# Kernel optimization log

Measured on AMD Instinct MI355X. Metric: run time of the kernel, lower is better.

Reference implementation:

```python
import jax, jax.numpy as jnp
import numpy as np

NUM_CLASSES = 80
IMG_DIM = 2048
WORD_DIM = 300
INTER = 1024


def _branch(fmap, word, W1, W2, W3, b3, Wa, ba):
    # fmap: [B, C, H, W] -> [B, H, W, C]  (matches torch transpose(1,2),(2,3))
    x = jnp.transpose(fmap, (0, 2, 3, 1))
    fw = jnp.einsum('bhwc,dc->bhwd', x, W1)          # [B,H,W,d]
    fd = jnp.einsum('kw,dw->kd', word, W2)            # [K,d]
    # broadcast instead of repeat: tanh-gated bilinear feature [B,H,W,K,d]
    t = jnp.tanh(fw[:, :, :, None, :] * fd[None, None, None, :, :])
    lb = jnp.einsum('bhwkd,ed->bhwke', t, W3) + b3    # [B,H,W,K,d]
    score = jnp.einsum('bhwkd,od->bhwko', lb, Wa)[..., 0] + ba[0]  # [B,H,W,K]
    B, H, W, K = score.shape
    coeff = jax.nn.softmax(score.reshape(B, H * W, K), axis=1).reshape(B, H, W, K)
    # weighted spatial sum pooling per class -> [B, K, C]
    return jnp.einsum('bhwk,bhwc->bkc', coeff, x)


def setup_inputs() -> dict:
    key = jax.random.key(0)
    ks = jax.random.split(key, 12)
    d2 = INTER // 2
    s = 0.02
    return {
        'batch_size': 4,
        'stage_3_img_feature_map': jax.random.normal(ks[0], (4, IMG_DIM // 2, 28, 28), jnp.float32),
        'stage_4_img_feature_map': jax.random.normal(ks[1], (4, IMG_DIM, 14, 14), jnp.float32),
        'word_features': jax.random.normal(ks[2], (NUM_CLASSES, WORD_DIM), jnp.float32),
        # stage-3 branch params (torch Linear weight layout [out, in])
        'W1_s3': jax.random.normal(ks[3], (d2, IMG_DIM // 2), jnp.float32) * s,
        'W2_s3': jax.random.normal(ks[4], (d2, WORD_DIM), jnp.float32) * s,
        'W3_s3': jax.random.normal(ks[5], (d2, d2), jnp.float32) * s,
        'b3_s3': jnp.zeros((d2,), jnp.float32),
        'Wa_s3': jax.random.normal(ks[6], (1, d2), jnp.float32) * s,
        'ba_s3': jnp.zeros((1,), jnp.float32),
        # stage-4 branch params
        'W1_s4': jax.random.normal(ks[7], (INTER, IMG_DIM), jnp.float32) * s,
        'W2_s4': jax.random.normal(ks[8], (INTER, WORD_DIM), jnp.float32) * s,
        'W3_s4': jax.random.normal(ks[9], (INTER, INTER), jnp.float32) * s,
        'b3_s4': jnp.zeros((INTER,), jnp.float32),
        'Wa_s4': jax.random.normal(ks[10], (1, INTER), jnp.float32) * s,
        'ba_s4': jnp.zeros((1,), jnp.float32),
    }


def reference(batch_size, stage_3_img_feature_map, stage_4_img_feature_map, word_features,
              W1_s3, W2_s3, W3_s3, b3_s3, Wa_s3, ba_s3,
              W1_s4, W2_s4, W3_s4, b3_s4, Wa_s4, ba_s4):
    out3 = _branch(stage_3_img_feature_map, word_features, W1_s3, W2_s3, W3_s3, b3_s3, Wa_s3, ba_s3)
    out4 = _branch(stage_4_img_feature_map, word_features, W1_s4, W2_s4, W3_s4, b3_s4, Wa_s4, ba_s4)
    return (out3, out4)
```

## Files before the change

kernel.cpp:

```cpp
#include <hip/hip_runtime.h>

#define K_CLS 80
#define WDIM  300

typedef __attribute__((ext_vector_type(8))) short s16x8;
typedef __attribute__((ext_vector_type(4))) short s16x4;
typedef __attribute__((ext_vector_type(4))) float f32x4;

__device__ inline unsigned short f2bf(float x) {
    unsigned int u = __builtin_bit_cast(unsigned int, x);
    unsigned int r = (u + 0x7fffu + ((u >> 16) & 1u)) >> 16;
    return (unsigned short)r;
}

__device__ inline float dot4(float4 a, float4 b) {
    return a.x * b.x + a.y * b.y + a.z * b.z + a.w * b.w;
}

__device__ inline float t4(float4 wv, float4 fv, float4 vv) {
    return vv.x * __builtin_amdgcn_rcpf(__builtin_amdgcn_exp2f(wv.x * fv.x) + 1.f)
         + vv.y * __builtin_amdgcn_rcpf(__builtin_amdgcn_exp2f(wv.y * fv.y) + 1.f)
         + vv.z * __builtin_amdgcn_rcpf(__builtin_amdgcn_exp2f(wv.z * fv.z) + 1.f)
         + vv.w * __builtin_amdgcn_rcpf(__builtin_amdgcn_exp2f(wv.w * fv.w) + 1.f);
}

__global__ __launch_bounds__(256) void k_small(
    const float* __restrict__ word,
    const float* __restrict__ W23, float* __restrict__ fd3,
    const float* __restrict__ W24, float* __restrict__ fd4,
    const float* __restrict__ Wa3, const float* __restrict__ W33, float* __restrict__ v3,
    const float* __restrict__ Wa4, const float* __restrict__ W34, float* __restrict__ v4) {
    __shared__ float red[4][64];
    int bid = blockIdx.x;
    int t = threadIdx.x;
    if (bid < 120) {
        const float* W2; float* fd; int D, kt, dblk;
        if (bid < 40) { W2 = W23; fd = fd3; D = 512; kt = bid >> 1; dblk = bid & 1; }
        else { int i2 = bid - 40; W2 = W24; fd = fd4; D = 1024; kt = i2 >> 2; dblk = i2 & 3; }
        int d = dblk * 256 + t;
        int k0 = kt * 4;
        const float4* w2p = (const float4*)(W2 + (size_t)d * WDIM);
        const float4* wr0 = (const float4*)(word + (size_t)(k0 + 0) * WDIM);
        const float4* wr1 = (const float4*)(word + (size_t)(k0 + 1) * WDIM);
        const float4* wr2 = (const float4*)(word + (size_t)(k0 + 2) * WDIM);
        const float4* wr3 = (const float4*)(word + (size_t)(k0 + 3) * WDIM);
        float a0 = 0.f, a1 = 0.f, a2 = 0.f, a3 = 0.f;
#pragma unroll 5
        for (int j = 0; j < WDIM / 4; ++j) {
            float4 w = w2p[j];
            a0 += dot4(wr0[j], w);
            a1 += dot4(wr1[j], w);
            a2 += dot4(wr2[j], w);
            a3 += dot4(wr3[j], w);
        }
        const float S = 2.885390081777927f;
        fd[(size_t)(k0 + 0) * D + d] = a0 * S;
        fd[(size_t)(k0 + 1) * D + d] = a1 * S;
        fd[(size_t)(k0 + 2) * D + d] = a2 * S;
        fd[(size_t)(k0 + 3) * D + d] = a3 * S;
    } else {
        const float* Wa; const float* W3; float* v; int D, vblk;
        if (bid < 128) { Wa = Wa3; W3 = W33; v = v3; D = 512; vblk = bid - 120; }
        else           { Wa = Wa4; W3 = W34; v = v4; D = 1024; vblk = bid - 128; }
        int d0 = vblk * 64;
        int dl = t & 63, eg = t >> 6;
        float a[8] = {};
        int nIt = D >> 5;
        for (int i = 0; i < nIt; ++i) {
            int e0 = eg + 32 * i;
#pragma unroll
            for (int j = 0; j < 8; ++j)
                a[j] = fmaf(Wa[e0 + 4 * j], W3[(size_t)(e0 + 4 * j) * D + d0 + dl], a[j]);
        }
        float s = ((a[0] + a[1]) + (a[2] + a[3])) + ((a[4] + a[5]) + (a[6] + a[7]));
        red[eg][dl] = s;
        __syncthreads();
        if (t < 64) v[d0 + t] = red[0][t] + red[1][t] + red[2][t] + red[3][t];
    }
}

__global__ __launch_bounds__(512) void k_fw(
    const float* __restrict__ fmap3, const float* __restrict__ W13, float* __restrict__ fw3,
    const float* __restrict__ fmap4, const float* __restrict__ W14, float* __restrict__ fw4) {
    __shared__ short Al[2][128 * 40];
    __shared__ short Bl[2][64 * 40];
    int gid = blockIdx.x;
    const float *fmap, *W1; float* fw; int C, HW, D, dnb, hwnb;
    if (gid < 224) { fmap = fmap3; W1 = W13; fw = fw3; C = 1024; HW = 784; D = 512;  dnb = 8;  hwnb = 7; }
    else { gid -= 224; fmap = fmap4; W1 = W14; fw = fw4; C = 2048; HW = 196; D = 1024; dnb = 16; hwnb = 2; }
    int dblk = gid % dnb; gid /= dnb;
    int hwblk = gid % hwnb;
    int b = gid / hwnb;
    int m0 = hwblk * 128, d0 = dblk * 64;
    int tid = threadIdx.x, wave = tid >> 6, lane = tid & 63;
    const float* fb = fmap + (size_t)b * C * HW;

    int am = tid & 127, ac0 = (tid >> 7) * 8;
    int bd = tid >> 3, bc0 = (tid & 7) * 4;
    int hwA = m0 + am;
    bool okA = hwA < HW;
    const float* aptr = fb + (size_t)ac0 * HW + (okA ? hwA : 0);
    const float* bptr = W1 + (size_t)(d0 + bd) * C + bc0;

    float ar[8];
    float4 br;
#pragma unroll
    for (int i = 0; i < 8; ++i) ar[i] = okA ? aptr[(size_t)i * HW] : 0.f;
    br = *(const float4*)bptr;

    f32x4 acc[4];
#pragma unroll
    for (int nr = 0; nr < 4; ++nr) acc[nr] = (f32x4){0.f, 0.f, 0.f, 0.f};

#define CW(bufi)                                                              \
    {                                                                         \
        s16x8 ap;                                                             \
        _Pragma("unroll") for (int i = 0; i < 8; ++i) ap[i] = (short)f2bf(ar[i]); \
        *(s16x8*)&Al[bufi][am * 40 + ac0] = ap;                               \
        s16x4 bp;                                                             \
        bp[0] = (short)f2bf(br.x); bp[1] = (short)f2bf(br.y);                 \
        bp[2] = (short)f2bf(br.z); bp[3] = (short)f2bf(br.w);                 \
        *(s16x4*)&Bl[bufi][bd * 40 + bc0] = bp;                               \
    }

    CW(0);
    __syncthreads();

    int NS = C >> 5;
    int ko = (lane >> 4) * 8, rr = lane & 15;
    for (int s = 0; s < NS; ++s) {
        if (s + 1 < NS) {
            const float* ap2 = aptr + (size_t)(s + 1) * 32 * HW;
#pragma unroll
            for (int i = 0; i < 8; ++i) ar[i] = okA ? ap2[(size_t)i * HW] : 0.f;
            br = *(const float4*)(bptr + (s + 1) * 32);
        }
        int buf = s & 1;
        s16x8 afr = *(s16x8*)&Al[buf][(wave * 16 + rr) * 40 + ko];
        s16x8 bfr[4];
#pragma unroll
        for (int nr = 0; nr < 4; ++nr)
            bfr[nr] = *(s16x8*)&Bl[buf][(nr * 16 + rr) * 40 + ko];
#pragma unroll
        for (int nr = 0; nr < 4; ++nr)
            acc[nr] = __builtin_amdgcn_mfma_f32_16x16x32_bf16(afr, bfr[nr], acc[nr], 0, 0, 0);
        if (s + 1 < NS) CW(buf ^ 1);
        __syncthreads();
    }
#undef CW

    int row4 = (lane >> 4) * 4, col = lane & 15;
#pragma unroll
    for (int j = 0; j < 4; ++j) {
        int mm = m0 + wave * 16 + row4 + j;
        if (mm < HW) {
#pragma unroll
            for (int nr = 0; nr < 4; ++nr)
                fw[((size_t)b * HW + mm) * D + d0 + nr * 16 + col] = acc[nr][j];
        }
    }
}

__global__ __launch_bounds__(320) void k_score(
    const float* __restrict__ fw3, const float* __restrict__ fd3,
    const float* __restrict__ v3, float* __restrict__ p3,
    const float* __restrict__ fw4, const float* __restrict__ fd4,
    const float* __restrict__ v4, float* __restrict__ p4) {
    __shared__ float fwl[4][1024];
    __shared__ float vl[1024];
    int bid = blockIdx.x;
    const float *fw, *fd, *v; float* p; int D, HW;
    if (bid < 784) { fw = fw3; fd = fd3; v = v3; p = p3; D = 512; HW = 784; }
    else { bid -= 784; fw = fw4; fd = fd4; v = v4; p = p4; D = 1024; HW = 196; }
    int nt = HW >> 2;
    int b = bid / nt, m0 = (bid - b * nt) * 4;
    int tid = threadIdx.x;
    const float* fwg = fw + ((size_t)b * HW + m0) * D;
    int D4 = D >> 2;
    if (tid < D4) {
        ((float4*)vl)[tid] = ((const float4*)v)[tid];
#pragma unroll
        for (int t = 0; t < 4; ++t)
            ((float4*)fwl[t])[tid] = ((const float4*)(fwg + (size_t)t * D))[tid];
    }
    __syncthreads();
    int wave = tid >> 6, lane = tid & 63;
    int kk = lane >> 2, ds = lane & 3;
    int k = wave * 16 + kk;
    const float4* fdp = (const float4*)(fd + (size_t)k * D);
    const float4* vp  = (const float4*)vl;
    const float4* w0p = (const float4*)fwl[0];
    const float4* w1p = (const float4*)fwl[1];
    const float4* w2p = (const float4*)fwl[2];
    const float4* w3p = (const float4*)fwl[3];
    float acc0 = 0.f, acc1 = 0.f, acc2 = 0.f, acc3 = 0.f;
    int NJ = D >> 4;
    for (int jj = 0; jj < NJ; jj += 2) {
        int c0 = jj * 4 + ds, c1 = c0 + 4;
        float4 f0 = fdp[c0], f1 = fdp[c1];
        float4 va = vp[c0], vb = vp[c1];
        acc0 += t4(w0p[c0], f0, va) + t4(w0p[c1], f1, vb);
        acc1 += t4(w1p[c0], f0, va) + t4(w1p[c1], f1, vb);
        acc2 += t4(w2p[c0], f0, va) + t4(w2p[c1], f1, vb);
        acc3 += t4(w3p[c0], f0, va) + t4(w3p[c1], f1, vb);
    }
    acc0 += __shfl_xor(acc0, 1); acc0 += __shfl_xor(acc0, 2);
    acc1 += __shfl_xor(acc1, 1); acc1 += __shfl_xor(acc1, 2);
    acc2 += __shfl_xor(acc2, 1); acc2 += __shfl_xor(acc2, 2);
    acc3 += __shfl_xor(acc3, 1); acc3 += __shfl_xor(acc3, 2);
    if (ds == 0) {
        const float S = -2.885390081777927f;
        float* pr = p + ((size_t)b * K_CLS + k) * HW + m0;
        pr[0] = __builtin_amdgcn_exp2f(acc0 * S);
        pr[1] = __builtin_amdgcn_exp2f(acc1 * S);
        pr[2] = __builtin_amdgcn_exp2f(acc2 * S);
        pr[3] = __builtin_amdgcn_exp2f(acc3 * S);
    }
}

#define CHUNK 128
__global__ __launch_bounds__(256) void k_pool(
    const float* __restrict__ p3, const float* __restrict__ fmap3,
    const float* __restrict__ p4, const float* __restrict__ fmap4,
    float* __restrict__ out) {
    __shared__ float pl[40][CHUNK];
    __shared__ float fl[32][CHUNK + 1];
    int bid = blockIdx.x;
    const float *p, *fmap; float* o; int C, HW;
    if (bid < 256) { p = p3; fmap = fmap3; o = out; C = 1024; HW = 784; }
    else { bid -= 256; p = p4; fmap = fmap4; o = out + (size_t)4 * K_CLS * 1024; C = 2048; HW = 196; }
    int cnb = C >> 5;
    int c0 = (bid % cnb) * 32; bid /= cnb;
    int kb = (bid & 1) * 40;
    int b = bid >> 1;
    int tid = threadIdx.x;
    int c_l = tid & 31;
    int k_l = (tid >> 5) * 5;
    const float* fb = fmap + (size_t)b * C * HW;
    float acc[5] = {}, ps[5] = {};
    for (int hw0 = 0; hw0 < HW; hw0 += CHUNK) {
        for (int idx = tid; idx < 40 * CHUNK; idx += 256) {
            int r = idx >> 7, cc = idx & (CHUNK - 1);
            int hw = hw0 + cc;
            pl[r][cc] = (hw < HW) ? p[((size_t)b * K_CLS + kb + r) * HW + hw] : 0.f;
        }
        for (int idx = tid; idx < 32 * CHUNK; idx += 256) {
            int r = idx >> 7, cc = idx & (CHUNK - 1);
            int hw = hw0 + cc;
            fl[r][cc] = (hw < HW) ? fb[(size_t)(c0 + r) * HW + hw] : 0.f;
        }
        __syncthreads();
#pragma unroll 4
        for (int j = 0; j < CHUNK; ++j) {
            float fv = fl[c_l][j];
#pragma unroll
            for (int t = 0; t < 5; ++t) {
                float pv = pl[k_l + t][j];
                acc[t] += pv * fv;
                ps[t] += pv;
            }
        }
        __syncthreads();
    }
#pragma unroll
    for (int t = 0; t < 5; ++t) {
        int k = kb + k_l + t;
        o[((size_t)b * K_CLS + k) * C + c0 + c_l] = acc[t] / ps[t];
    }
}

extern "C" void kernel_launch(void* const* d_in, const int* in_sizes, int n_in,
                              void* d_out, int out_size, void* d_ws, size_t ws_size,
                              hipStream_t stream) {
    const float* fmap3 = (const float*)d_in[1];
    const float* fmap4 = (const float*)d_in[2];
    const float* word  = (const float*)d_in[3];
    const float* W1_3  = (const float*)d_in[4];
    const float* W2_3  = (const float*)d_in[5];
    const float* W3_3  = (const float*)d_in[6];
    const float* Wa_3  = (const float*)d_in[8];
    const float* W1_4  = (const float*)d_in[10];
    const float* W2_4  = (const float*)d_in[11];
    const float* W3_4  = (const float*)d_in[12];
    const float* Wa_4  = (const float*)d_in[14];
    float* out = (float*)d_out;

    float* ws = (float*)d_ws;
    size_t off = 0;
    float* fw3 = ws + off; off += (size_t)3136 * 512;
    float* fd3 = ws + off; off += (size_t)80 * 512;
    float* v3  = ws + off; off += 512;
    float* sc3 = ws + off; off += (size_t)4 * 80 * 784;
    float* fw4 = ws + off; off += (size_t)784 * 1024;
    float* fd4 = ws + off; off += (size_t)80 * 1024;
    float* v4  = ws + off; off += 1024;
    float* sc4 = ws + off; off += (size_t)4 * 80 * 196;

    k_small<<<144, 256, 0, stream>>>(word, W2_3, fd3, W2_4, fd4,
                                     Wa_3, W3_3, v3, Wa_4, W3_4, v4);
    k_fw<<<352, 512, 0, stream>>>(fmap3, W1_3, fw3, fmap4, W1_4, fw4);
    k_score<<<980, 320, 0, stream>>>(fw3, fd3, v3, sc3, fw4, fd4, v4, sc4);
    k_pool<<<768, 256, 0, stream>>>(sc3, fmap3, sc4, fmap4, out);
}
```

Baseline: 315.6 us.

## Move softmax denominator into score kernel via atomics and widen pool tiles

The score kernel now writes its four exp values as one float4 and atomically adds their sum into a per-(batch,class) denominator, which an extra block in k_small zeroes first. With the denominator precomputed, the pool kernel drops its running sums. Each pool block now covers 64 channels over 64-position chunks using float4 loads from global and shared memory, which halves the grid and reuses each loaded p value across two channels. The cost is atomic contention in the score kernel and fewer pool blocks to spread across the GPU.

After: 294.9 us. -6.6%, faster.

```diff
diff --git a/kernel.cpp b/kernel.cpp
--- a/kernel.cpp
+++ b/kernel.cpp
@@ -29,7 +29,8 @@
     const float* __restrict__ W23, float* __restrict__ fd3,
     const float* __restrict__ W24, float* __restrict__ fd4,
     const float* __restrict__ Wa3, const float* __restrict__ W33, float* __restrict__ v3,
-    const float* __restrict__ Wa4, const float* __restrict__ W34, float* __restrict__ v4) {
+    const float* __restrict__ Wa4, const float* __restrict__ W34, float* __restrict__ v4,
+    float* __restrict__ ps3, float* __restrict__ ps4) {
     __shared__ float red[4][64];
     int bid = blockIdx.x;
     int t = threadIdx.x;
@@ -58,7 +59,7 @@
         fd[(size_t)(k0 + 1) * D + d] = a1 * S;
         fd[(size_t)(k0 + 2) * D + d] = a2 * S;
         fd[(size_t)(k0 + 3) * D + d] = a3 * S;
-    } else {
+    } else if (bid < 144) {
         const float* Wa; const float* W3; float* v; int D, vblk;
         if (bid < 128) { Wa = Wa3; W3 = W33; v = v3; D = 512; vblk = bid - 120; }
         else           { Wa = Wa4; W3 = W34; v = v4; D = 1024; vblk = bid - 128; }
@@ -76,6 +77,8 @@
         red[eg][dl] = s;
         __syncthreads();
         if (t < 64) v[d0 + t] = red[0][t] + red[1][t] + red[2][t] + red[3][t];
+    } else {
+        for (int i = t; i < 4 * K_CLS; i += 256) { ps3[i] = 0.f; ps4[i] = 0.f; }
     }
 }
 
@@ -163,15 +166,15 @@
 
 __global__ __launch_bounds__(320) void k_score(
     const float* __restrict__ fw3, const float* __restrict__ fd3,
-    const float* __restrict__ v3, float* __restrict__ p3,
+    const float* __restrict__ v3, float* __restrict__ p3, float* __restrict__ ps3,
     const float* __restrict__ fw4, const float* __restrict__ fd4,
-    const float* __restrict__ v4, float* __restrict__ p4) {
+    const float* __restrict__ v4, float* __restrict__ p4, float* __restrict__ ps4) {
     __shared__ float fwl[4][1024];
     __shared__ float vl[1024];
     int bid = blockIdx.x;
-    const float *fw, *fd, *v; float* p; int D, HW;
-    if (bid < 784) { fw = fw3; fd = fd3; v = v3; p = p3; D = 512; HW = 784; }
-    else { bid -= 784; fw = fw4; fd = fd4; v = v4; p = p4; D = 1024; HW = 196; }
+    const float *fw, *fd, *v; float *p, *psum; int D, HW;
+    if (bid < 784) { fw = fw3; fd = fd3; v = v3; p = p3; psum = ps3; D = 512; HW = 784; }
+    else { bid -= 784; fw = fw4; fd = fd4; v = v4; p = p4; psum = ps4; D = 1024; HW = 196; }
     int nt = HW >> 2;
     int b = bid / nt, m0 = (bid - b * nt) * 4;
     int tid = threadIdx.x;
@@ -210,54 +213,64 @@
     acc3 += __shfl_xor(acc3, 1); acc3 += __shfl_xor(acc3, 2);
     if (ds == 0) {
         const float S = -2.885390081777927f;
-        float* pr = p + ((size_t)b * K_CLS + k) * HW + m0;
-        pr[0] = __builtin_amdgcn_exp2f(acc0 * S);
-        pr[1] = __builtin_amdgcn_exp2f(acc1 * S);
-        pr[2] = __builtin_amdgcn_exp2f(acc2 * S);
-        pr[3] = __builtin_amdgcn_exp2f(acc3 * S);
-    }
-}
-
-#define CHUNK 128
+        float4 pv;
+        pv.x = __builtin_amdgcn_exp2f(acc0 * S);
+        pv.y = __builtin_amdgcn_exp2f(acc1 * S);
+        pv.z = __builtin_amdgcn_exp2f(acc2 * S);
+        pv.w = __builtin_amdgcn_exp2f(acc3 * S);
+        *(float4*)(p + ((size_t)b * K_CLS + k) * HW + m0) = pv;
+        atomicAdd(&psum[b * K_CLS + k], (pv.x + pv.y) + (pv.z + pv.w));
+    }
+}
+
+#define PCH 64
 __global__ __launch_bounds__(256) void k_pool(
     const float* __restrict__ p3, const float* __restrict__ fmap3,
+    const float* __restrict__ ps3,
     const float* __restrict__ p4, const float* __restrict__ fmap4,
-    float* __restrict__ out) {
-    __shared__ float pl[40][CHUNK];
-    __shared__ float fl[32][CHUNK + 1];
+    const float* __restrict__ ps4, float* __restrict__ out) {
+    __shared__ float pl[40][PCH + 4];
+    __shared__ float fl[64][PCH + 4];
     int bid = blockIdx.x;
-    const float *p, *fmap; float* o; int C, HW;
-    if (bid < 256) { p = p3; fmap = fmap3; o = out; C = 1024; HW = 784; }
-    else { bid -= 256; p = p4; fmap = fmap4; o = out + (size_t)4 * K_CLS * 1024; C = 2048; HW = 196; }
-    int cnb = C >> 5;
-    int c0 = (bid % cnb) * 32; bid /= cnb;
+    const float *p, *fmap, *psum; float* o; int C, HW, cnb;
+    if (bid < 128) { p = p3; fmap = fmap3; psum = ps3; o = out; C = 1024; HW = 784; cnb = 16; }
+    else { bid -= 128; p = p4; fmap = fmap4; psum = ps4; o = out + (size_t)4 * K_CLS * 1024; C = 2048; HW = 196; cnb = 32; }
+    int c0 = (bid % cnb) * 64; bid /= cnb;
     int kb = (bid & 1) * 40;
     int b = bid >> 1;
     int tid = threadIdx.x;
-    int c_l = tid & 31;
-    int k_l = (tid >> 5) * 5;
-    const float* fb = fmap + (size_t)b * C * HW;
-    float acc[5] = {}, ps[5] = {};
-    for (int hw0 = 0; hw0 < HW; hw0 += CHUNK) {
-        for (int idx = tid; idx < 40 * CHUNK; idx += 256) {
-            int r = idx >> 7, cc = idx & (CHUNK - 1);
+    int cg = tid & 31, kg = tid >> 5;
+    int k_l = kg * 5;
+    const float* fb = fmap + ((size_t)b * C + c0) * HW;
+    const float* pb = p + ((size_t)b * K_CLS + kb) * HW;
+    float acc[5][2] = {};
+    int nch = (HW + PCH - 1) / PCH;
+    for (int ch = 0; ch < nch; ++ch) {
+        int hw0 = ch * PCH;
+        for (int i = tid; i < 40 * (PCH / 4); i += 256) {
+            int r = i >> 4, cc = (i & 15) * 4;
             int hw = hw0 + cc;
-            pl[r][cc] = (hw < HW) ? p[((size_t)b * K_CLS + kb + r) * HW + hw] : 0.f;
-        }
-        for (int idx = tid; idx < 32 * CHUNK; idx += 256) {
-            int r = idx >> 7, cc = idx & (CHUNK - 1);
+            float4 val = (hw < HW) ? *(const float4*)(pb + (size_t)r * HW + hw)
+                                   : make_float4(0.f, 0.f, 0.f, 0.f);
+            *(float4*)&pl[r][cc] = val;
+        }
+        for (int i = tid; i < 64 * (PCH / 4); i += 256) {
+            int r = i >> 4, cc = (i & 15) * 4;
             int hw = hw0 + cc;
-            fl[r][cc] = (hw < HW) ? fb[(size_t)(c0 + r) * HW + hw] : 0.f;
+            float4 val = (hw < HW) ? *(const float4*)(fb + (size_t)r * HW + hw)
+                                   : make_float4(0.f, 0.f, 0.f, 0.f);
+            *(float4*)&fl[r][cc] = val;
         }
         __syncthreads();
 #pragma unroll 4
-        for (int j = 0; j < CHUNK; ++j) {
-            float fv = fl[c_l][j];
+        for (int jj = 0; jj < PCH / 4; ++jj) {
+            float4 fa = *(const float4*)&fl[cg][jj * 4];
+            float4 fbv = *(const float4*)&fl[cg + 32][jj * 4];
 #pragma unroll
             for (int t = 0; t < 5; ++t) {
-                float pv = pl[k_l + t][j];
-                acc[t] += pv * fv;
-                ps[t] += pv;
+                float4 pv = *(const float4*)&pl[k_l + t][jj * 4];
+                acc[t][0] += dot4(pv, fa);
+                acc[t][1] += dot4(pv, fbv);
             }
         }
         __syncthreads();
@@ -265,7 +278,10 @@
 #pragma unroll
     for (int t = 0; t < 5; ++t) {
         int k = kb + k_l + t;
-        o[((size_t)b * K_CLS + k) * C + c0 + c_l] = acc[t] / ps[t];
+        float inv = 1.0f / psum[b * K_CLS + k];
+        float* orow = o + ((size_t)b * K_CLS + k) * C + c0;
+        orow[cg] = acc[t][0] * inv;
+        orow[cg + 32] = acc[t][1] * inv;
     }
 }
 
@@ -295,10 +311,12 @@
     float* fd4 = ws + off; off += (size_t)80 * 1024;
     float* v4  = ws + off; off += 1024;
     float* sc4 = ws + off; off += (size_t)4 * 80 * 196;
-
-    k_small<<<144, 256, 0, stream>>>(word, W2_3, fd3, W2_4, fd4,
-                                     Wa_3, W3_3, v3, Wa_4, W3_4, v4);
+    float* ps3 = ws + off; off += 320;
+    float* ps4 = ws + off; off += 320;
+
+    k_small<<<145, 256, 0, stream>>>(word, W2_3, fd3, W2_4, fd4,
+                                     Wa_3, W3_3, v3, Wa_4, W3_4, v4, ps3, ps4);
     k_fw<<<352, 512, 0, stream>>>(fmap3, W1_3, fw3, fmap4, W1_4, fw4);
-    k_score<<<980, 320, 0, stream>>>(fw3, fd3, v3, sc3, fw4, fd4, v4, sc4);
-    k_pool<<<768, 256, 0, stream>>>(sc3, fmap3, sc4, fmap4, out);
-}
+    k_score<<<980, 320, 0, stream>>>(fw3, fd3, v3, sc3, ps3, fw4, fd4, v4, sc4, ps4);
+    k_pool<<<384, 256, 0, stream>>>(sc3, fmap3, ps3, sc4, fmap4, ps4, out);
+}
```
